# Kernel tuning notes

Hardware: AMD Instinct MI355X
Metric: run time of the kernel (lower is better)

Reference implementation:

```python
import jax, jax.numpy as jnp
import numpy as np

DIM = 96
RES = (8, 56, 56)
WIN = (8, 7, 7)
SHIFT = (4, 3, 3)
HEADS = (3, 6)
EPS = 1e-5


def _rel_pos_index(wd, wh, ww):
    coords = np.stack(np.meshgrid(np.arange(wd), np.arange(wh), np.arange(ww), indexing='ij'))
    cf = coords.reshape(3, -1)                       # (3, N)
    rel = (cf[:, :, None] - cf[:, None, :]).transpose(1, 2, 0)  # (N, N, 3)
    rel[..., 0] += wd - 1
    rel[..., 1] += wh - 1
    rel[..., 2] += ww - 1
    rel[..., 0] *= (2 * wh - 1) * (2 * ww - 1)
    rel[..., 1] *= (2 * ww - 1)
    return rel.sum(-1)                               # (N, N) int


def _attn_mask(D, H, W, win, shift):
    wd, wh, ww = win
    sd, sh, sw = shift
    img = np.zeros((D, H, W), np.float32)
    cnt = 0
    for ds in (slice(0, -wd), slice(-wd, -sd), slice(-sd, None)):
        for hs in (slice(0, -wh), slice(-wh, -sh), slice(-sh, None)):
            for vs in (slice(0, -ww), slice(-ww, -sw), slice(-sw, None)):
                img[ds, hs, vs] = cnt
                cnt += 1
    m = img.reshape(D // wd, wd, H // wh, wh, W // ww, ww)
    m = m.transpose(0, 2, 4, 1, 3, 5).reshape(-1, wd * wh * ww)   # (nW, N)
    diff = m[:, None, :] - m[:, :, None]
    return np.where(diff != 0, np.float32(-100.0), np.float32(0.0))


def _ln_c(x, w, b):
    # LayerNorm over the channel dim of (B,C,D,H,W)
    mu = x.mean(axis=1, keepdims=True)
    var = ((x - mu) ** 2).mean(axis=1, keepdims=True)
    xn = (x - mu) * jax.lax.rsqrt(var + EPS)
    return xn * w[None, :, None, None, None] + b[None, :, None, None, None]


def _window_partition(x, win):
    B, C, D, H, W = x.shape
    wd, wh, ww = win
    x = x.transpose(0, 2, 3, 4, 1)
    x = x.reshape(B, D // wd, wd, H // wh, wh, W // ww, ww, C)
    x = x.transpose(0, 1, 3, 5, 2, 4, 6, 7)
    return x.reshape(-1, wd * wh * ww, C)            # (B*nW, N, C)


def _window_reverse(w, win, B, D, H, W):
    wd, wh, ww = win
    C = w.shape[-1]
    x = w.reshape(B, D // wd, H // wh, W // ww, wd, wh, ww, C)
    x = x.transpose(0, 1, 4, 2, 5, 3, 6, 7).reshape(B, D, H, W, C)
    return x.transpose(0, 4, 1, 2, 3)


def _win_attn(xw, mask, rel_idx, qkv_w, qkv_b, proj_w, proj_b, rpb, h):
    Bn, N, C = xw.shape
    dh = C // h
    qkv = (xw @ qkv_w.T + qkv_b).reshape(Bn, N, 3, h, dh).transpose(2, 0, 3, 1, 4)
    q, k, v = qkv[0], qkv[1], qkv[2]                 # (Bn, h, N, dh)
    attn = jnp.einsum('bhnd,bhmd->bhnm', q * (dh ** -0.5), k)
    bias = rpb[rel_idx.reshape(-1)].reshape(N, N, h).transpose(2, 0, 1)
    attn = attn + bias[None]
    nW = mask.shape[0]
    attn = (attn.reshape(Bn // nW, nW, h, N, N) + mask[None, :, None]).reshape(Bn, h, N, N)
    attn = jax.nn.softmax(attn, axis=-1)
    out = jnp.einsum('bhnm,bhmd->bhnd', attn, v).transpose(0, 2, 1, 3).reshape(Bn, N, C)
    return out @ proj_w.T + proj_b


def _conv3d(x, w, b, groups=1):
    y = jax.lax.conv_general_dilated(x, w, (1, 1, 1), 'SAME',
                                     dimension_numbers=('NCDHW', 'OIDHW', 'NCDHW'),
                                     feature_group_count=groups)
    return y + b[None, :, None, None, None]


def setup_inputs() -> dict:
    key = jax.random.key(0)
    ks = jax.random.split(key, 16)
    C = DIM
    s = 0.02
    inp = {
        'x': jax.random.normal(ks[0], (2, C, *RES), jnp.float32),
        'ln1_w': jnp.ones((C,), jnp.float32), 'ln1_b': jnp.zeros((C,), jnp.float32),
        'ln2_w': jnp.ones((C,), jnp.float32), 'ln2_b': jnp.zeros((C,), jnp.float32),
        'qkv_w0': jax.random.normal(ks[1], (3 * C, C), jnp.float32) * s,
        'qkv_b0': jnp.zeros((3 * C,), jnp.float32),
        'proj_w0': jax.random.normal(ks[2], (C, C), jnp.float32) * s,
        'proj_b0': jnp.zeros((C,), jnp.float32),
        'rpb0': jax.random.normal(ks[3], (15 * 13 * 13, HEADS[0]), jnp.float32) * s,
        'qkv_w1': jax.random.normal(ks[4], (3 * C, C), jnp.float32) * s,
        'qkv_b1': jnp.zeros((3 * C,), jnp.float32),
        'proj_w1': jax.random.normal(ks[5], (C, C), jnp.float32) * s,
        'proj_b1': jnp.zeros((C,), jnp.float32),
        'rpb1': jax.random.normal(ks[6], (15 * 13 * 13, HEADS[1]), jnp.float32) * s,
        'alpha_attn': jax.random.normal(ks[7], (2,), jnp.float32),
        'conv3_w': jax.random.normal(ks[8], (C, C, 3, 3, 3), jnp.float32) * s,
        'conv3_b': jnp.zeros((C,), jnp.float32),
        'conv1_w': jax.random.normal(ks[9], (C, C, 1, 1, 1), jnp.float32) * s,
        'conv1_b': jnp.zeros((C,), jnp.float32),
        'dw_w': jax.random.normal(ks[10], (C, 1, 3, 3, 3), jnp.float32) * s,
        'dw_b': jnp.zeros((C,), jnp.float32),
        'alpha_ffn': jax.random.normal(ks[11], (4,), jnp.float32),
    }
    return inp


def reference(x, ln1_w, ln1_b, ln2_w, ln2_b,
              qkv_w0, qkv_b0, proj_w0, proj_b0, rpb0,
              qkv_w1, qkv_b1, proj_w1, proj_b1, rpb1,
              alpha_attn, conv3_w, conv3_b, conv1_w, conv1_b, dw_w, dw_b, alpha_ffn):
    B, C, D, H, W = x.shape
    sd, sh, sw = SHIFT
    mask = jnp.asarray(_attn_mask(D, H, W, WIN, SHIFT))     # (nW, N, N), constant
    rel_idx = jnp.asarray(_rel_pos_index(*WIN))             # (N, N), constant

    # --- attention branch (soft NAS mixture) ---
    xn = _ln_c(x, ln1_w, ln1_b)
    shifted = jnp.roll(xn, (-sd, -sh, -sw), axis=(2, 3, 4))
    win = _window_partition(shifted, WIN)
    aw = jax.nn.softmax(alpha_attn)
    a0 = _win_attn(win, mask, rel_idx, qkv_w0, qkv_b0, proj_w0, proj_b0, rpb0, HEADS[0])
    a1 = _win_attn(win, mask, rel_idx, qkv_w1, qkv_b1, proj_w1, proj_b1, rpb1, HEADS[1])
    attn_out = aw[0] * a0 + aw[1] * a1
    xr = _window_reverse(attn_out, WIN, B, D, H, W)
    x_attn = jnp.roll(xr, (sd, sh, sw), axis=(2, 3, 4))
    x1 = x + x_attn                                         # gate=None -> 1.0, drop_path=0

    # --- FFN branch (soft NAS mixture of conv ops) ---
    x2 = _ln_c(x1, ln2_w, ln2_b)
    fw = jax.nn.softmax(alpha_ffn)
    ffn = (fw[0] * _conv3d(x2, conv3_w, conv3_b)
           + fw[1] * _conv3d(x2, conv1_w, conv1_b)
           + fw[2] * _conv3d(x2, dw_w, dw_b, groups=C)
           + fw[3] * x2)
    return x1 + ffn
```

## Files before the change

kernel.cpp:

```cpp
#include <hip/hip_runtime.h>

#define NWIN 128
#define NTOK 392
#define SPAT 25088
#define NELEM 4816896

typedef unsigned short u16t;
typedef unsigned int u32t;
typedef __attribute__((ext_vector_type(8))) short short8;
typedef __attribute__((ext_vector_type(4))) float f32x4;

#define PW 58
#define PHW 3364
#define PSPAT 33640
#define XPAD_U16 6458880
#define WCOMB_N 248832
#define WPROJ_N 18432
#define NTOKTOT 50176
#define LOG2E 1.44269504f

__device__ __forceinline__ unsigned int f2bf(float f) {
  unsigned int u = __float_as_uint(f);
  return (u + 0x7fffu + ((u >> 16) & 1u)) >> 16;
}
__device__ __forceinline__ unsigned int pack2(float a, float b) {
  return f2bf(a) | (f2bf(b) << 16);
}
__device__ __forceinline__ u32t cvtpk(float lo, float hi) {
  u32t r;
  asm("v_cvt_pk_bf16_f32 %0, %1, %2" : "=v"(r) : "v"(lo), "v"(hi));
  return r;
}
__device__ __forceinline__ float exp2v(float x) {
  return __builtin_amdgcn_exp2f(x);
}
__device__ __forceinline__ float bflo(unsigned int u) { return __uint_as_float(u << 16); }

__global__ __launch_bounds__(128)
void k_ln1_win(const float* __restrict__ x, const float* __restrict__ lw,
               const float* __restrict__ lb, u16t* __restrict__ xw) {
  __shared__ float s1[128], s2[128];
  int t = blockIdx.x;
  int win = t / NTOK, n = t % NTOK;
  int b = win >> 6, wrem = win & 63;
  int hwin = wrem >> 3, wwin = wrem & 7;
  int ld = n / 49, r = n % 49, lh = r / 7, lw2 = r % 7;
  int d = (ld + 4) & 7;
  int h = (hwin * 7 + lh + 3) % 56;
  int w = (wwin * 7 + lw2 + 3) % 56;
  size_t base = (size_t)b * 96 * SPAT + d * 3136 + h * 56 + w;
  int c = threadIdx.x;
  float v = (c < 96) ? x[base + (size_t)c * SPAT] : 0.f;
  s1[c] = v; s2[c] = v * v;
  __syncthreads();
  #pragma unroll
  for (int st = 64; st > 0; st >>= 1) {
    if (c < st) { s1[c] += s1[c + st]; s2[c] += s2[c + st]; }
    __syncthreads();
  }
  float mu = s1[0] * (1.f / 96.f);
  float var = s2[0] * (1.f / 96.f) - mu * mu;
  float rs = rsqrtf(var + 1e-5f);
  if (c < 96) xw[(size_t)t * 96 + c] = (u16t)f2bf((v - mu) * rs * lw[c] + lb[c]);
}

__global__ __launch_bounds__(256)
void k_qprep(const float* __restrict__ w0, const float* __restrict__ w1,
             u16t* __restrict__ wq) {
  int e = blockIdx.x * 256 + threadIdx.x;
  if (e >= 2 * 27648) return;
  wq[e] = (u16t)f2bf(e < 27648 ? w0[e] : w1[e - 27648]);
}

template<int DH>
__global__ __launch_bounds__(256)
void k_qkv_mfma(const u16t* __restrict__ xw, const u16t* __restrict__ wq,
                const float* __restrict__ bias, u16t* __restrict__ qkvh) {
  int tid = threadIdx.x;
  int lane = tid & 63, wv = tid >> 6;
  int c = lane & 15, lg = lane >> 4;
  int t = blockIdx.x * 64 + wv * 16 + c;
  const u16t* bp = xw + (size_t)t * 96 + lg * 8;
  short8 bv[3];
  #pragma unroll
  for (int kc = 0; kc < 3; ++kc)
    bv[kc] = *reinterpret_cast<const short8*>(bp + kc * 32);
  f32x4 acc[18];
  #pragma unroll
  for (int f = 0; f < 18; ++f) acc[f] = (f32x4){0.f, 0.f, 0.f, 0.f};
  #pragma unroll
  for (int kc = 0; kc < 3; ++kc) {
    #pragma unroll
    for (int f = 0; f < 18; ++f) {
      short8 av = *reinterpret_cast<const short8*>(
          wq + (size_t)(f * 16 + c) * 96 + kc * 32 + lg * 8);
      acc[f] = __builtin_amdgcn_mfma_f32_16x16x32_bf16(av, bv[kc], acc[f], 0, 0, 0);
    }
  }
  #pragma unroll
  for (int f = 0; f < 18; ++f) {
    int co = f * 16 + lg * 4;
    float4 bb = *reinterpret_cast<const float4*>(bias + co);
    uint2 st = make_uint2(pack2(acc[f][0] + bb.x, acc[f][1] + bb.y),
                          pack2(acc[f][2] + bb.z, acc[f][3] + bb.w));
    int sel = co / 96, rem = co % 96;
    int head = rem / DH, dh = rem % DH;
    *reinterpret_cast<uint2*>(qkvh + (size_t)sel * NTOKTOT * 96
        + (size_t)head * NTOKTOT * DH + (size_t)t * DH + dh) = st;
  }
}

template<int H>
__global__ __launch_bounds__(256)
void k_rprep(const float* __restrict__ rpb, u16t* __restrict__ rpbc) {
  int e = blockIdx.x * 256 + threadIdx.x;
  if (e >= H * 2536) return;
  int h = e / 2536, idx = e % 2536;
  rpbc[e] = (idx < 2535) ? (u16t)f2bf(rpb[idx * H + h] * LOG2E) : (u16t)0;
}

template<int H, int DH>
__global__ __launch_bounds__(512, (DH == 16) ? 6 : 4)
void k_attn_mfma(const u16t* __restrict__ qkvh, const u16t* __restrict__ rpbc,
                 u16t* __restrict__ aout) {
  constexpr float SCALE2 = ((DH == 32) ? 0.17677669529663689f : 0.25f) * LOG2E;
  constexpr float MASKV = -100.f * LOG2E;
  constexpr float THR = 8.f * LOG2E;
  constexpr int NT = DH / 16;
  constexpr int QSPLIT = (DH == 16) ? 1 : 2;
  constexpr int KROW = (DH == 32) ? 32 : 16;
  constexpr int KS_U16 = (DH == 32) ? (416 * 32) : (417 * 16);
  constexpr int BLK = 512;
  __shared__ __align__(16) u16t Ks[KS_U16];
  __shared__ __align__(16) u16t VTs[DH * 424];
  __shared__ u16t rpbs[2536];
  __shared__ u16t Ts[416];
  __shared__ u32t RGp[104];

  int bid = blockIdx.x;
  int xcd = bid & 7, i = bid >> 3;
  int win = xcd * 16 + (i & 15);
  int hp = i >> 4;
  int head = (DH == 32) ? (hp >> 1) : hp;
  int part = (DH == 32) ? (hp & 1) : 0;
  int wrem = win & 63;
  int hwin = wrem >> 3, wwin = wrem & 7;
  int tid = threadIdx.x;
  int lane = tid & 63, wv = tid >> 6;
  int c = lane & 15, lg = lane >> 4;

  const u16t* qh = qkvh + (size_t)head * NTOKTOT * DH + (size_t)win * NTOK * DH;
  const u16t* kh = qh + (size_t)NTOKTOT * 96;
  const u16t* vh = qh + (size_t)2 * NTOKTOT * 96;
  u16t* ao = aout + (size_t)head * NTOKTOT * DH + (size_t)win * NTOK * DH;

  {
    uint4 z = make_uint4(0u, 0u, 0u, 0u);
    uint4* k4 = (uint4*)Ks;
    for (int i2 = tid; i2 < KS_U16 / 8; i2 += BLK) k4[i2] = z;
    uint4* v4 = (uint4*)VTs;
    for (int i2 = tid; i2 < (DH * 424) / 8; i2 += BLK) v4[i2] = z;
  }
  __syncthreads();
  constexpr int DG = DH / 8;
  for (int u = tid; u < NTOK * DG; u += BLK) {
    int j = u / DG, dg = u % DG;
    uint4 kv = *reinterpret_cast<const uint4*>(kh + (size_t)j * DH + dg * 8);
    int sch = (DH == 32) ? (dg ^ (j & 3)) : (dg ^ ((j & 1) ^ ((j >> 2) & 1)));
    *reinterpret_cast<uint4*>(&Ks[j * KROW + sch * 8]) = kv;
    union { uint4 q; u16t s[8]; } vv;
    vv.q = *reinterpret_cast<const uint4*>(vh + (size_t)j * DH + dg * 8);
    #pragma unroll
    for (int ee = 0; ee < 8; ++ee) VTs[(dg * 8 + ee) * 424 + j] = vv.s[ee];
  }
  for (int i2 = tid; i2 < 2536; i2 += BLK) rpbs[i2] = rpbc[head * 2536 + i2];
  for (int j = tid; j < 416; j += BLK) {
    u16t tv = 0;
    if (j < NTOK) {
      int ld = j / 49, r = j % 49, lh = r / 7, lw = r % 7;
      tv = (u16t)(ld * 169 + lh * 13 + lw);
    }
    Ts[j] = tv;
  }
  for (int j4 = tid; j4 < 104; j4 += BLK) {
    u32t w = 0;
    #pragma unroll
    for (int bb = 0; bb < 4; ++bb) {
      int j = j4 * 4 + bb;
      u32t rg = 255;
      if (j < NTOK) {
        int ld = j / 49, r = j % 49, lh = r / 7, lw = r % 7;
        int hpp = hwin * 7 + lh, wpp = wwin * 7 + lw;
        int rd = (ld < 4) ? 1 : 2;
        int rh = (hpp < 49) ? 0 : ((hpp < 53) ? 1 : 2);
        int rw = (wpp < 49) ? 0 : ((wpp < 53) ? 1 : 2);
        rg = (u32t)(rd * 9 + rh * 3 + rw);
      }
      w |= rg << (8 * bb);
    }
    RGp[j4] = w;
  }
  __syncthreads();

  constexpr int QBASE = 25 / QSPLIT;
  constexpr int QREM = 25 % QSPLIT;
  int q0 = part * QBASE + ((part < QREM) ? part : QREM);
  int q1 = q0 + QBASE + ((part < QREM) ? 1 : 0);

  for (int qt = q0 + wv; qt < q1; qt += 8) {
    int qtok = qt * 16 + c;
    int qcl = (qtok < NTOK) ? qtok : NTOK - 1;
    int Tq = (int)Ts[qcl] + 1267;
    u32t rgq = (RGp[qcl >> 2] >> ((qcl & 3) * 8)) & 255u;
    short8 bq;
    {
      const u16t* qp = qh + (size_t)qcl * DH;
      union { u32t u[4]; short8 v; } bu;
      #pragma unroll
      for (int i2 = 0; i2 < 4; ++i2) {
        u16t e0 = (DH == 32 || lg < 2) ? qp[lg * 8 + 2 * i2] : (u16t)0;
        u16t e1 = (DH == 32 || lg < 2) ? qp[lg * 8 + 2 * i2 + 1] : (u16t)0;
        bu.u[i2] = (u32t)e0 | ((u32t)e1 << 16);
      }
      bq = bu.v;
    }
    float m = -1e30f, lsum = 0.f;
    f32x4 oacc[NT];
    #pragma unroll
    for (int ot = 0; ot < NT; ++ot) oacc[ot] = (f32x4){0.f, 0.f, 0.f, 0.f};
    int srcl = ((lane >> 4) & 1) * 32 + c;
    #pragma unroll 1
    for (int tt = 0; tt < 13; ++tt) {
      f32x4 p0, p1;
      #pragma unroll
      for (int half = 0; half < 2; ++half) {
        int t = 2 * tt + half;
        int addr;
        if (DH == 32) {
          addr = (16 * t + c) * 32 + ((lg ^ (c & 3)) * 8);
        } else {
          int fc = (c & 1) ^ ((c >> 2) & 1);
          addr = (lg < 2) ? ((16 * t + c) * 16 + (((lg & 1) ^ fc) * 8)) : (416 * 16);
        }
        short8 av = *reinterpret_cast<const short8*>(&Ks[addr]);
        f32x4 a = (f32x4){0.f, 0.f, 0.f, 0.f};
        a = __builtin_amdgcn_mfma_f32_16x16x32_bf16(av, bq, a, 0, 0, 0);
        int kb = 16 * t + lg * 4;
        const u32t* tsp = reinterpret_cast<const u32t*>(&Ts[kb]);
        u32t tsa = tsp[0], tsb = tsp[1];
        u32t rgw = RGp[4 * t + lg];
        f32x4 p;
        p[0] = a[0] * SCALE2 + bflo((u32t)rpbs[Tq - (int)(tsa & 0xffffu)])
             + ((((rgw      ) & 255u) != rgq) ? MASKV : 0.f);
        p[1] = a[1] * SCALE2 + bflo((u32t)rpbs[Tq - (int)(tsa >> 16)])
             + ((((rgw >>  8) & 255u) != rgq) ? MASKV : 0.f);
        p[2] = a[2] * SCALE2 + bflo((u32t)rpbs[Tq - (int)(tsb & 0xffffu)])
             + ((((rgw >> 16) & 255u) != rgq) ? MASKV : 0.f);
        p[3] = a[3] * SCALE2 + bflo((u32t)rpbs[Tq - (int)(tsb >> 16)])
             + ((((rgw >> 24)        ) != rgq) ? MASKV : 0.f);
        if (half == 0) p0 = p; else p1 = p;
      }
      float pm = fmaxf(fmaxf(fmaxf(p0[0], p0[1]), fmaxf(p0[2], p0[3])),
                       fmaxf(fmaxf(p1[0], p1[1]), fmaxf(p1[2], p1[3])));
      pm = fmaxf(pm, __shfl_xor(pm, 16));
      pm = fmaxf(pm, __shfl_xor(pm, 32));
      bool dead = (pm <= m - 25.f) || (pm <= -90.f);
      if (__all(dead)) continue;
      if (!__all(pm <= m + THR)) {
        float mnew = fmaxf(pm, m);
        float fac = exp2v(m - mnew);
        lsum *= fac;
        #pragma unroll
        for (int ot = 0; ot < NT; ++ot) oacc[ot] *= fac;
        m = mnew;
      }
      #pragma unroll
      for (int j = 0; j < 4; ++j) {
        p0[j] = exp2v(p0[j] - m);
        p1[j] = exp2v(p1[j] - m);
      }
      lsum += p0[0] + p0[1] + p0[2] + p0[3] + p1[0] + p1[1] + p1[2] + p1[3];
      u32t pk0x = cvtpk(p0[0], p0[1]);
      u32t pk0y = cvtpk(p0[2], p0[3]);
      u32t pk1x = cvtpk(p1[0], p1[1]);
      u32t pk1y = cvtpk(p1[2], p1[3]);
      u32t ax = (u32t)__shfl((int)pk0x, srcl),      ay = (u32t)__shfl((int)pk0y, srcl);
      u32t bx = (u32t)__shfl((int)pk0x, srcl + 16), by = (u32t)__shfl((int)pk0y, srcl + 16);
      u32t cx = (u32t)__shfl((int)pk1x, srcl),      cy = (u32t)__shfl((int)pk1y, srcl);
      u32t dx = (u32t)__shfl((int)pk1x, srcl + 16), dy = (u32t)__shfl((int)pk1y, srcl + 16);
      bool hi = (lane & 32) != 0;
      union { u32t u[4]; short8 v; } au;
      au.u[0] = hi ? cx : ax; au.u[1] = hi ? cy : ay;
      au.u[2] = hi ? dx : bx; au.u[3] = hi ? dy : by;
      #pragma unroll
      for (int ot = 0; ot < NT; ++ot) {
        short8 bv = *reinterpret_cast<const short8*>(
            &VTs[(ot * 16 + c) * 424 + 32 * tt + lg * 8]);
        oacc[ot] = __builtin_amdgcn_mfma_f32_16x16x32_bf16(au.v, bv, oacc[ot], 0, 0, 0);
      }
    }
    lsum += __shfl_xor(lsum, 16);
    lsum += __shfl_xor(lsum, 32);
    float inv = 1.f / lsum;
    float invj[4];
    #pragma unroll
    for (int j = 0; j < 4; ++j) invj[j] = __shfl(inv, lg * 4 + j);
    #pragma unroll
    for (int j = 0; j < 4; ++j) {
      int q = qt * 16 + lg * 4 + j;
      if (q < NTOK) {
        #pragma unroll
        for (int ot = 0; ot < NT; ++ot)
          ao[(size_t)q * DH + ot * 16 + c] = (u16t)f2bf(oacc[ot][j] * invj[j]);
      }
    }
  }
}

__global__ __launch_bounds__(256)
void k_pprep(const float* __restrict__ pw0, const float* __restrict__ pb0,
             const float* __restrict__ pw1, const float* __restrict__ pb1,
             const float* __restrict__ alpha,
             u16t* __restrict__ wp, float* __restrict__ bp) {
  int e = blockIdx.x * 256 + threadIdx.x;
  if (e >= WPROJ_N) return;
  float al0 = alpha[0], al1 = alpha[1];
  float m = fmaxf(al0, al1);
  float e0 = expf(al0 - m), e1 = expf(al1 - m);
  float aw0 = e0 / (e0 + e1), aw1 = e1 / (e0 + e1);
  int co = e / 192, k = e % 192;
  float v = (k < 96) ? aw0 * pw0[co * 96 + k] : aw1 * pw1[co * 96 + k - 96];
  wp[e] = (u16t)f2bf(v);
  if (e < 96) bp[e] = aw0 * pb0[e] + aw1 * pb1[e];
}

__global__ __launch_bounds__(64)
void k_proj_mfma(const u16t* __restrict__ a0, const u16t* __restrict__ a1,
                 const u16t* __restrict__ wp, const float* __restrict__ bp,
                 const float* __restrict__ x, float* __restrict__ x1) {
  int lane = threadIdx.x;
  int c = lane & 15, lg = lane >> 4;
  int t = blockIdx.x * 16 + c;
  int win = t / NTOK, n = t % NTOK;
  int b = win >> 6, wrem = win & 63;
  int hwin = wrem >> 3, wwin = wrem & 7;
  int ld = n / 49, r = n % 49, lh = r / 7, lw = r % 7;
  int d = (ld + 4) & 7;
  int h = (hwin * 7 + lh + 3) % 56;
  int w = (wwin * 7 + lw + 3) % 56;
  size_t base = (size_t)b * 96 * SPAT + d * 3136 + h * 56 + w;

  f32x4 acc[6];
  #pragma unroll
  for (int f = 0; f < 6; ++f) acc[f] = (f32x4){0.f, 0.f, 0.f, 0.f};
  #pragma unroll
  for (int kc = 0; kc < 6; ++kc) {
    short8 bv;
    if (kc < 3) {
      bv = *reinterpret_cast<const short8*>(a0 + ((size_t)kc * NTOKTOT + t) * 32 + lg * 8);
    } else {
      int h1 = (kc - 3) * 2 + (lg >> 1);
      bv = *reinterpret_cast<const short8*>(a1 + ((size_t)h1 * NTOKTOT + t) * 16 + (lg & 1) * 8);
    }
    #pragma unroll
    for (int f = 0; f < 6; ++f) {
      short8 av = *reinterpret_cast<const short8*>(wp + (f * 16 + c) * 192 + kc * 32 + lg * 8);
      acc[f] = __builtin_amdgcn_mfma_f32_16x16x32_bf16(av, bv, acc[f], 0, 0, 0);
    }
  }
  #pragma unroll
  for (int f = 0; f < 6; ++f) {
    #pragma unroll
    for (int j = 0; j < 4; ++j) {
      int co = f * 16 + lg * 4 + j;
      size_t idx = base + (size_t)co * SPAT;
      x1[idx] = x[idx] + acc[f][j] + bp[co];
    }
  }
}

__global__ __launch_bounds__(256)
void k_zero(uint4* __restrict__ p, int n) {
  int i = blockIdx.x * 256 + threadIdx.x;
  if (i < n) p[i] = make_uint4(0u, 0u, 0u, 0u);
}

__global__ __launch_bounds__(256)
void k_wprep(const float* __restrict__ c3w, const float* __restrict__ c3b,
             const float* __restrict__ c1w, const float* __restrict__ c1b,
             const float* __restrict__ dww, const float* __restrict__ dwb,
             const float* __restrict__ alpha,
             u16t* __restrict__ wcomb, float* __restrict__ bcomb) {
  int e = blockIdx.x * 256 + threadIdx.x;
  if (e >= WCOMB_N) return;
  float a0 = alpha[0], a1 = alpha[1], a2 = alpha[2], a3 = alpha[3];
  float mx = fmaxf(fmaxf(a0, a1), fmaxf(a2, a3));
  float e0 = expf(a0 - mx), e1 = expf(a1 - mx), e2 = expf(a2 - mx), e3 = expf(a3 - mx);
  float inv = 1.f / (e0 + e1 + e2 + e3);
  float f0 = e0 * inv, f1 = e1 * inv, f2 = e2 * inv, f3 = e3 * inv;
  int ko = e / 9216, rm = e % 9216, co = rm / 96, ci = rm % 96;
  float v = f0 * c3w[(co * 96 + ci) * 27 + ko];
  if (ko == 13) v += f1 * c1w[co * 96 + ci];
  if (ci == co) v += f2 * dww[co * 27 + ko];
  if (ko == 13 && ci == co) v += f3;
  wcomb[e] = (u16t)f2bf(v);
  if (e < 96) bcomb[e] = f0 * c3b[e] + f1 * c1b[e] + f2 * dwb[e];
}

__global__ __launch_bounds__(256)
void k_ln2pad(const float* __restrict__ x1, const float* __restrict__ lw,
              const float* __restrict__ lb, u16t* __restrict__ xpad) {
  int p = blockIdx.x * 256 + threadIdx.x;
  int b = p / SPAT, s = p % SPAT;
  int d = s / 3136, r = s % 3136, h = r / 56, w = r % 56;
  const float* xp = x1 + (size_t)b * 96 * SPAT + s;
  float sum = 0.f, sq = 0.f;
  #pragma unroll 8
  for (int c = 0; c < 96; ++c) {
    float v = xp[(size_t)c * SPAT];
    sum += v; sq += v * v;
  }
  float mu = sum * (1.f / 96.f);
  float var = sq * (1.f / 96.f) - mu * mu;
  float rs = rsqrtf(var + 1e-5f);
  int psp = ((b * 10 + d + 1) * 58 + (h + 1)) * 58 + (w + 1);
  u16t* op = xpad + (size_t)psp * 96;
  #pragma unroll
  for (int g = 0; g < 12; ++g) {
    float v0 = xp[(size_t)(8 * g + 0) * SPAT], v1 = xp[(size_t)(8 * g + 1) * SPAT];
    float v2 = xp[(size_t)(8 * g + 2) * SPAT], v3 = xp[(size_t)(8 * g + 3) * SPAT];
    float v4 = xp[(size_t)(8 * g + 4) * SPAT], v5 = xp[(size_t)(8 * g + 5) * SPAT];
    float v6 = xp[(size_t)(8 * g + 6) * SPAT], v7 = xp[(size_t)(8 * g + 7) * SPAT];
    uint4 st;
    st.x = pack2((v0 - mu) * rs * lw[8*g+0] + lb[8*g+0], (v1 - mu) * rs * lw[8*g+1] + lb[8*g+1]);
    st.y = pack2((v2 - mu) * rs * lw[8*g+2] + lb[8*g+2], (v3 - mu) * rs * lw[8*g+3] + lb[8*g+3]);
    st.z = pack2((v4 - mu) * rs * lw[8*g+4] + lb[8*g+4], (v5 - mu) * rs * lw[8*g+5] + lb[8*g+5]);
    st.w = pack2((v6 - mu) * rs * lw[8*g+6] + lb[8*g+6], (v7 - mu) * rs * lw[8*g+7] + lb[8*g+7]);
    *reinterpret_cast<uint4*>(op + g * 8) = st;
  }
}

__global__ __launch_bounds__(256)
void k_ffn_mfma(const u16t* __restrict__ xpad, const u16t* __restrict__ wcomb,
                const float* __restrict__ bcomb, float* __restrict__ out) {
  __shared__ __align__(16) u16t wls[2][96 * 104];
  int tid = threadIdx.x;
  int lane = tid & 63, wv = tid >> 6;
  int fh = wv >> 1;
  int sh = wv & 1;
  int c = lane & 15, kg = lane >> 4;
  int bid = blockIdx.x;
  int swz = (bid & 7) * 98 + (bid >> 3);
  int pbase[2], obase[2];
  #pragma unroll
  for (int nt = 0; nt < 2; ++nt) {
    int m = swz * 64 + sh * 32 + nt * 16 + c;
    int b = m / SPAT, r = m % SPAT;
    int d = r / 3136, r2 = r % 3136, h = r2 / 56, w = r2 % 56;
    int psp0 = ((b * 10 + d) * 58 + h) * 58 + w;
    pbase[nt] = psp0 * 96 + kg * 8;
    obase[nt] = b * (96 * SPAT) + r;
  }
  f32x4 acc[2][3];
  #pragma unroll
  for (int nt = 0; nt < 2; ++nt)
    #pragma unroll
    for (int ff = 0; ff < 3; ++ff) acc[nt][ff] = (f32x4){0.f, 0.f, 0.f, 0.f};

  {
    const uint4* src = (const uint4*)(wcomb);
    for (int e = tid; e < 1152; e += 256) {
      uint4 v = src[e];
      int co = (e * 8) / 96, ci = (e * 8) % 96;
      *reinterpret_cast<uint4*>(&wls[0][co * 104 + ci]) = v;
    }
  }
  __syncthreads();
  int buf = 0;
  for (int ko = 0; ko < 27; ++ko) {
    int kd = ko / 9, kh = (ko / 3) % 3, kw = ko % 3;
    int tapoff = (kd * PHW + kh * PW + kw) * 96;
    if (ko + 1 < 27) {
      const uint4* src = (const uint4*)(wcomb + (ko + 1) * 9216);
      for (int e = tid; e < 1152; e += 256) {
        uint4 v = src[e];
        int co = (e * 8) / 96, ci = (e * 8) % 96;
        *reinterpret_cast<uint4*>(&wls[buf ^ 1][co * 104 + ci]) = v;
      }
    }
    #pragma unroll
    for (int cc = 0; cc < 3; ++cc) {
      short8 bv[2];
      #pragma unroll
      for (int nt = 0; nt < 2; ++nt)
        bv[nt] = *reinterpret_cast<const short8*>(xpad + pbase[nt] + tapoff + cc * 32);
      #pragma unroll
      for (int ff = 0; ff < 3; ++ff) {
        short8 av = *reinterpret_cast<const short8*>(
            &wls[buf][((fh * 3 + ff) * 16 + c) * 104 + cc * 32 + kg * 8]);
        acc[0][ff] = __builtin_amdgcn_mfma_f32_16x16x32_bf16(av, bv[0], acc[0][ff], 0, 0, 0);
        acc[1][ff] = __builtin_amdgcn_mfma_f32_16x16x32_bf16(av, bv[1], acc[1][ff], 0, 0, 0);
      }
    }
    __syncthreads();
    buf ^= 1;
  }
  #pragma unroll
  for (int nt = 0; nt < 2; ++nt)
    #pragma unroll
    for (int ff = 0; ff < 3; ++ff)
      #pragma unroll
      for (int j = 0; j < 4; ++j) {
        int co = (fh * 3 + ff) * 16 + kg * 4 + j;
        float* o = out + obase[nt] + co * SPAT;
        *o = *o + acc[nt][ff][j] + bcomb[co];
      }
}

extern "C" void kernel_launch(void* const* d_in, const int* in_sizes, int n_in,
                              void* d_out, int out_size, void* d_ws, size_t ws_size,
                              hipStream_t stream) {
  (void)in_sizes; (void)n_in; (void)out_size; (void)ws_size;
  const float* x      = (const float*)d_in[0];
  const float* ln1w   = (const float*)d_in[1];
  const float* ln1b   = (const float*)d_in[2];
  const float* ln2w   = (const float*)d_in[3];
  const float* ln2b   = (const float*)d_in[4];
  const float* qkvw0  = (const float*)d_in[5];
  const float* qkvb0  = (const float*)d_in[6];
  const float* projw0 = (const float*)d_in[7];
  const float* projb0 = (const float*)d_in[8];
  const float* rpb0   = (const float*)d_in[9];
  const float* qkvw1  = (const float*)d_in[10];
  const float* qkvb1  = (const float*)d_in[11];
  const float* projw1 = (const float*)d_in[12];
  const float* projb1 = (const float*)d_in[13];
  const float* rpb1   = (const float*)d_in[14];
  const float* aattn  = (const float*)d_in[15];
  const float* c3w    = (const float*)d_in[16];
  const float* c3b    = (const float*)d_in[17];
  const float* c1w    = (const float*)d_in[18];
  const float* c1b    = (const float*)d_in[19];
  const float* dww    = (const float*)d_in[20];
  const float* dwb    = (const float*)d_in[21];
  const float* affn   = (const float*)d_in[22];

  u16t* u    = (u16t*)d_ws;
  u16t* xw   = u;
  u16t* a0   = xw + (size_t)NTOKTOT * 96;
  u16t* a1   = a0 + (size_t)3 * NTOKTOT * 32;
  u16t* qkvh = a1 + (size_t)6 * NTOKTOT * 16;
  u16t* wq   = qkvh + (size_t)3 * NTOKTOT * 96;
  u16t* rpbc0 = wq + 2 * 27648;
  u16t* rpbc1 = rpbc0 + 3 * 2536;
  u16t* xpad  = qkvh;
  u16t* wcomb = xpad + XPAD_U16;
  float* bcomb = (float*)(wcomb + WCOMB_N);
  u16t* wproj = (u16t*)(bcomb + 96);
  float* bproj = (float*)(wproj + WPROJ_N);
  float* x1  = (float*)d_out;

  k_ln1_win<<<NWIN * NTOK, 128, 0, stream>>>(x, ln1w, ln1b, xw);
  k_qprep<<<216, 256, 0, stream>>>(qkvw0, qkvw1, wq);
  k_rprep<3><<<30, 256, 0, stream>>>(rpb0, rpbc0);
  k_rprep<6><<<60, 256, 0, stream>>>(rpb1, rpbc1);
  k_qkv_mfma<32><<<784, 256, 0, stream>>>(xw, wq, qkvb0, qkvh);
  k_attn_mfma<3, 32><<<768, 512, 0, stream>>>(qkvh, rpbc0, a0);
  k_qkv_mfma<16><<<784, 256, 0, stream>>>(xw, wq + 27648, qkvb1, qkvh);
  k_attn_mfma<6, 16><<<768, 512, 0, stream>>>(qkvh, rpbc1, a1);
  k_zero<<<(XPAD_U16 / 8 + 255) / 256, 256, 0, stream>>>((uint4*)xpad, XPAD_U16 / 8);
  k_wprep<<<(WCOMB_N + 255) / 256, 256, 0, stream>>>(c3w, c3b, c1w, c1b, dww, dwb,
                                                     affn, wcomb, bcomb);
  k_pprep<<<(WPROJ_N + 255) / 256, 256, 0, stream>>>(projw0, projb0, projw1, projb1,
                                                     aattn, wproj, bproj);
  k_proj_mfma<<<3136, 64, 0, stream>>>(a0, a1, wproj, bproj, x, x1);
  k_ln2pad<<<196, 256, 0, stream>>>(x1, ln2w, ln2b, xpad);
  k_ffn_mfma<<<784, 256, 0, stream>>>(xpad, wcomb, bcomb, (float*)d_out);
}
```

Baseline: 317.1 us.

## Split FFN conv kernel across output-channel halves to double grid size

The 3D conv MFMA kernel now assigns each block one half of the output channels (48) over 64 spatial positions, with each wave covering 16 positions, instead of all 96 channels. The grid doubles to 1568 blocks and per-block LDS for staged weights halves, which should raise occupancy and spread work across more CUs. In exchange, each input activation tile is loaded from global memory twice (once per channel half), and each wave gets less MFMA work per LDS weight read.

```diff
diff --git a/kernel.cpp b/kernel.cpp
--- a/kernel.cpp
+++ b/kernel.cpp
@@ -443,36 +443,31 @@
 __global__ __launch_bounds__(256)
 void k_ffn_mfma(const u16t* __restrict__ xpad, const u16t* __restrict__ wcomb,
                 const float* __restrict__ bcomb, float* __restrict__ out) {
-  __shared__ __align__(16) u16t wls[2][96 * 104];
+  __shared__ __align__(16) u16t wls[2][48 * 104];
   int tid = threadIdx.x;
   int lane = tid & 63, wv = tid >> 6;
-  int fh = wv >> 1;
-  int sh = wv & 1;
   int c = lane & 15, kg = lane >> 4;
   int bid = blockIdx.x;
-  int swz = (bid & 7) * 98 + (bid >> 3);
-  int pbase[2], obase[2];
-  #pragma unroll
-  for (int nt = 0; nt < 2; ++nt) {
-    int m = swz * 64 + sh * 32 + nt * 16 + c;
-    int b = m / SPAT, r = m % SPAT;
-    int d = r / 3136, r2 = r % 3136, h = r2 / 56, w = r2 % 56;
-    int psp0 = ((b * 10 + d) * 58 + h) * 58 + w;
-    pbase[nt] = psp0 * 96 + kg * 8;
-    obase[nt] = b * (96 * SPAT) + r;
-  }
-  f32x4 acc[2][3];
-  #pragma unroll
-  for (int nt = 0; nt < 2; ++nt)
-    #pragma unroll
-    for (int ff = 0; ff < 3; ++ff) acc[nt][ff] = (f32x4){0.f, 0.f, 0.f, 0.f};
+  int coh = bid & 1;
+  int sp = bid >> 1;
+  int swz = (sp & 7) * 98 + (sp >> 3);
+  int m = swz * 64 + wv * 16 + c;
+  int b = m / SPAT, r = m % SPAT;
+  int d = r / 3136, r2 = r % 3136, h = r2 / 56, w = r2 % 56;
+  int psp0 = ((b * 10 + d) * 58 + h) * 58 + w;
+  int pbase = psp0 * 96 + kg * 8;
+  int obase = b * (96 * SPAT) + r;
+
+  f32x4 acc[3];
+  #pragma unroll
+  for (int ff = 0; ff < 3; ++ff) acc[ff] = (f32x4){0.f, 0.f, 0.f, 0.f};
 
   {
-    const uint4* src = (const uint4*)(wcomb);
-    for (int e = tid; e < 1152; e += 256) {
+    const uint4* src = (const uint4*)(wcomb) + coh * 576;
+    for (int e = tid; e < 576; e += 256) {
       uint4 v = src[e];
-      int co = (e * 8) / 96, ci = (e * 8) % 96;
-      *reinterpret_cast<uint4*>(&wls[0][co * 104 + ci]) = v;
+      int lco = (e * 8) / 96, ci = (e * 8) % 96;
+      *reinterpret_cast<uint4*>(&wls[0][lco * 104 + ci]) = v;
     }
   }
   __syncthreads();
@@ -481,40 +476,34 @@
     int kd = ko / 9, kh = (ko / 3) % 3, kw = ko % 3;
     int tapoff = (kd * PHW + kh * PW + kw) * 96;
     if (ko + 1 < 27) {
-      const uint4* src = (const uint4*)(wcomb + (ko + 1) * 9216);
-      for (int e = tid; e < 1152; e += 256) {
+      const uint4* src = (const uint4*)(wcomb) + (ko + 1) * 1152 + coh * 576;
+      for (int e = tid; e < 576; e += 256) {
         uint4 v = src[e];
-        int co = (e * 8) / 96, ci = (e * 8) % 96;
-        *reinterpret_cast<uint4*>(&wls[buf ^ 1][co * 104 + ci]) = v;
+        int lco = (e * 8) / 96, ci = (e * 8) % 96;
+        *reinterpret_cast<uint4*>(&wls[buf ^ 1][lco * 104 + ci]) = v;
       }
     }
     #pragma unroll
     for (int cc = 0; cc < 3; ++cc) {
-      short8 bv[2];
-      #pragma unroll
-      for (int nt = 0; nt < 2; ++nt)
-        bv[nt] = *reinterpret_cast<const short8*>(xpad + pbase[nt] + tapoff + cc * 32);
+      short8 bv = *reinterpret_cast<const short8*>(xpad + pbase + tapoff + cc * 32);
       #pragma unroll
       for (int ff = 0; ff < 3; ++ff) {
         short8 av = *reinterpret_cast<const short8*>(
-            &wls[buf][((fh * 3 + ff) * 16 + c) * 104 + cc * 32 + kg * 8]);
-        acc[0][ff] = __builtin_amdgcn_mfma_f32_16x16x32_bf16(av, bv[0], acc[0][ff], 0, 0, 0);
-        acc[1][ff] = __builtin_amdgcn_mfma_f32_16x16x32_bf16(av, bv[1], acc[1][ff], 0, 0, 0);
+            &wls[buf][(ff * 16 + c) * 104 + cc * 32 + kg * 8]);
+        acc[ff] = __builtin_amdgcn_mfma_f32_16x16x32_bf16(av, bv, acc[ff], 0, 0, 0);
       }
     }
     __syncthreads();
     buf ^= 1;
   }
   #pragma unroll
-  for (int nt = 0; nt < 2; ++nt)
-    #pragma unroll
-    for (int ff = 0; ff < 3; ++ff)
-      #pragma unroll
-      for (int j = 0; j < 4; ++j) {
-        int co = (fh * 3 + ff) * 16 + kg * 4 + j;
-        float* o = out + obase[nt] + co * SPAT;
-        *o = *o + acc[nt][ff][j] + bcomb[co];
-      }
+  for (int ff = 0; ff < 3; ++ff)
+    #pragma unroll
+    for (int j = 0; j < 4; ++j) {
+      int co = coh * 48 + ff * 16 + kg * 4 + j;
+      float* o = out + obase + co * SPAT;
+      *o = *o + acc[ff][j] + bcomb[co];
+    }
 }
 
 extern "C" void kernel_launch(void* const* d_in, const int* in_sizes, int n_in,
@@ -575,5 +564,5 @@
                                                      aattn, wproj, bproj);
   k_proj_mfma<<<3136, 64, 0, stream>>>(a0, a1, wproj, bproj, x, x1);
   k_ln2pad<<<196, 256, 0, stream>>>(x1, ln2w, ln2b, xpad);
-  k_ffn_mfma<<<784, 256, 0, stream>>>(xpad, wcomb, bcomb, (float*)d_out);
-}
+  k_ffn_mfma<<<1568, 256, 0, stream>>>(xpad, wcomb, bcomb, (float*)d_out);
+}
```

New measurement: 305.5 us. -3.6%, faster.
